# Performance work log

Hardware: AMD Instinct MI355X
Metric: run time of the kernel (lower is better)

Reference implementation:

```python
import jax, jax.numpy as jnp
import numpy as np

D_MODEL = 256
D_INNER = 512          # expand * d_model
HEADDIM = 64
NHEADS = D_INNER // HEADDIM   # 8
NGROUPS = 1
D_STATE = 64
D_IN_PROJ = 2 * D_INNER + 2 * NGROUPS * D_STATE + NHEADS   # 1160
CONV_DIM = D_INNER + 2 * NGROUPS * D_STATE                  # 640
LN_EPS = 1e-5


def setup_inputs() -> dict:
    key = jax.random.key(0)
    ks = jax.random.split(key, 16)
    s = 0.02
    # dt_bias init as in torch code
    dt = jnp.exp(jax.random.uniform(ks[10], (NHEADS,)) * (np.log(0.1) - np.log(0.001)) + np.log(0.001))
    dt = jnp.clip(dt, 1e-4)
    dt_bias = dt + jnp.log(-jnp.expm1(-dt))
    A_log = jnp.log(jax.random.uniform(ks[11], (NHEADS,), minval=1.0, maxval=16.0))
    return {
        "u": jax.random.normal(ks[0], (4, 8192, D_MODEL), dtype=jnp.float32),
        "H": 64,
        "W": 128,
        "W_in": jax.random.normal(ks[1], (D_IN_PROJ, D_MODEL), dtype=jnp.float32) * s,
        "W_stereo": jax.random.normal(ks[2], (D_IN_PROJ, D_INNER), dtype=jnp.float32) * s,
        "conv_l_w": jax.random.normal(ks[3], (CONV_DIM, 1, 3, 3), dtype=jnp.float32) * 0.1,
        "conv_l_b": jax.random.normal(ks[4], (CONV_DIM,), dtype=jnp.float32) * 0.01,
        "conv_r_w": jax.random.normal(ks[5], (CONV_DIM, 1, 3, 3), dtype=jnp.float32) * 0.1,
        "conv_r_b": jax.random.normal(ks[6], (CONV_DIM,), dtype=jnp.float32) * 0.01,
        "conv_w": jax.random.normal(ks[7], (CONV_DIM, 1, 3, 3), dtype=jnp.float32) * 0.1,
        "conv_b": jax.random.normal(ks[8], (CONV_DIM,), dtype=jnp.float32) * 0.01,
        "dt_bias": dt_bias,
        "A_log": A_log,
        "D_l": jnp.ones((NHEADS,), dtype=jnp.float32),
        "D_r": jnp.ones((NHEADS,), dtype=jnp.float32),
        "D": jnp.ones((NHEADS,), dtype=jnp.float32),
        "ln_g": jnp.ones((D_INNER,), dtype=jnp.float32),
        "ln_b": jnp.zeros((D_INNER,), dtype=jnp.float32),
        "W_out": jax.random.normal(ks[9], (D_MODEL, D_INNER), dtype=jnp.float32) * s,
    }


def _dwconv(x, w, b):
    # x: (B, C, H, W); depthwise 3x3 conv, SAME padding ((d_conv-1)//2 = 1)
    y = jax.lax.conv_general_dilated(
        x, w, window_strides=(1, 1), padding='SAME',
        dimension_numbers=('NCHW', 'OIHW', 'NCHW'),
        feature_group_count=CONV_DIM)
    return y + b[None, :, None, None]


def _layernorm(x, g, b):
    mu = x.mean(-1, keepdims=True)
    var = x.var(-1, keepdims=True)
    return (x - mu) / jnp.sqrt(var + LN_EPS) * g + b


def _lin_attn(x, dt, A, Bm, Cm, Dp):
    # x: (b, l, d_inner), dt: (b, l, h), Bm/Cm: (b, l, d_state); ngroups == 1
    b, l, _ = x.shape
    xh = x.reshape(b, l, NHEADS, HEADDIM)              # V: (b, l, h, p)
    dA = -(dt[..., None] * A[None, None, :, None])     # ssd_positve_dA -> -dt*A, (b,l,h,1)
    KV = jnp.einsum('bls,blhp->bhsp', Bm, xh * dA)     # K^T @ V_scaled
    y = jnp.einsum('bls,bhsp->blhp', Cm, KV)           # Q @ KV
    y = y + xh * Dp[None, None, :, None]               # skip D
    return y.reshape(b, l, D_INNER)


def reference(u, H, W, W_in, W_stereo, conv_l_w, conv_l_b, conv_r_w, conv_r_b,
              conv_w, conv_b, dt_bias, A_log, D_l, D_r, D, ln_g, ln_b, W_out):
    batch, seqlen, _ = u.shape
    half = batch // 2
    silu = jax.nn.silu
    A = -jnp.exp(A_log)

    zxbcdt = u @ W_in.T                                             # (b, l, 1160)
    z, xBC, dt = jnp.split(zxbcdt, [D_INNER, D_INNER + CONV_DIM], axis=-1)
    dt = jax.nn.softplus(dt + dt_bias)                              # (b, l, h)

    xBC = xBC.reshape(batch, H, W, CONV_DIM).transpose(0, 3, 1, 2)  # NCHW
    xBC1 = silu(_dwconv(xBC[:half], conv_l_w, conv_l_b)).transpose(0, 2, 3, 1).reshape(half, H * W, CONV_DIM)
    xBC2 = silu(_dwconv(xBC[half:], conv_r_w, conv_r_b)).transpose(0, 2, 3, 1).reshape(half, H * W, CONV_DIM)

    x1, B1, C1 = jnp.split(xBC1, [D_INNER, D_INNER + NGROUPS * D_STATE], axis=-1)
    x2, B2, C2 = jnp.split(xBC2, [D_INNER, D_INNER + NGROUPS * D_STATE], axis=-1)
    dt1, dt2 = dt[:half], dt[half:]

    y1 = _layernorm(_lin_attn(x1, dt1, A, B1, C1, D_l), ln_g, ln_b)
    y2 = _layernorm(_lin_attn(x2, dt2, A, B2, C2, D_r), ln_g, ln_b)
    y = jnp.concatenate([y1, y2], axis=0) * z

    zxs = y @ W_stereo.T
    zs, xBCs, dts = jnp.split(zxs, [D_INNER, D_INNER + CONV_DIM], axis=-1)
    dts = jax.nn.softplus(dts + dt_bias)

    xBCs = xBCs.reshape(batch, H, W, CONV_DIM).transpose(0, 3, 1, 2)
    xBCs = silu(_dwconv(xBCs, conv_w, conv_b)).transpose(0, 2, 3, 1).reshape(batch, H * W, CONV_DIM)
    xs, Bs, Cs = jnp.split(xBCs, [D_INNER, D_INNER + NGROUPS * D_STATE], axis=-1)

    ys = _layernorm(_lin_attn(xs, dts, A, Bs, Cs, D), ln_g, ln_b) * zs
    return ys @ W_out.T
```

## Files before the change

kernel.cpp:

```cpp
#include <hip/hip_runtime.h>
#include <hip/hip_bf16.h>
#include <math.h>

#define NB    4
#define LSEQ  8192
#define HH    64
#define WW    128
#define DMODEL 256
#define DINNER 512
#define NH    8
#define DSTATE 64
#define DPROJ 1160
#define CONVD 640
#define MROWS (NB*LSEQ)
#define KVCH  32
#define CBLK  80

typedef unsigned short bf16_t;
typedef __attribute__((ext_vector_type(8))) unsigned short ushort8v;
typedef __attribute__((ext_vector_type(8))) short short8v;
typedef __attribute__((ext_vector_type(4))) float f32x4;

static __device__ __forceinline__ float bf2f(bf16_t u) {
    return __uint_as_float(((unsigned)u) << 16);
}
static __device__ __forceinline__ bf16_t f2bf(float f) {
    unsigned u = __float_as_uint(f);
    u += 0x7FFFu + ((u >> 16) & 1u);
    return (bf16_t)(u >> 16);
}

template <typename TC>
__global__ __launch_bounds__(256) void gemm_mfma_bt(
    const bf16_t* __restrict__ A, int lda, size_t sAb,
    const bf16_t* __restrict__ B, int ldb, size_t sBb,
    TC* __restrict__ C, int ldc, size_t sCb,
    int M, int N, int K)
{
    __shared__ __align__(16) bf16_t As[128 * 32];
    __shared__ __align__(16) bf16_t Bs[128 * 32];
    const bf16_t* Ab = A + blockIdx.z * sAb;
    const bf16_t* Bb = B + blockIdx.z * sBb;
    TC*            Cb = C + blockIdx.z * sCb;
    const int tid = threadIdx.x;
    const int m0 = blockIdx.y * 128;
    const int n0 = blockIdx.x * 128;
    const int wid = tid >> 6;
    const int lane = tid & 63;
    const int wr = (wid >> 1) * 64;
    const int wc = (wid & 1) * 64;
    const int fr = lane & 15;
    const int fk = (lane >> 4) * 8;

    f32x4 acc[4][4];
    #pragma unroll
    for (int i = 0; i < 4; ++i)
        #pragma unroll
        for (int j = 0; j < 4; ++j) acc[i][j] = (f32x4){0.f, 0.f, 0.f, 0.f};

    const int srow = tid >> 2;
    const int scol = (tid & 3) * 8;
    const bf16_t* gA = Ab + (size_t)(m0 + srow) * lda + scol;
    const bf16_t* gB = Bb + (size_t)(n0 + srow) * ldb + scol;
    bf16_t* lA = As + tid * 8;
    bf16_t* lB = Bs + tid * 8;

    for (int k0 = 0; k0 < K; k0 += 32) {
        __builtin_amdgcn_global_load_lds(
            (const __attribute__((address_space(1))) void*)(gA + k0),
            (__attribute__((address_space(3))) void*)lA, 16, 0, 0);
        __builtin_amdgcn_global_load_lds(
            (const __attribute__((address_space(1))) void*)(gA + (size_t)64 * lda + k0),
            (__attribute__((address_space(3))) void*)(lA + 2048), 16, 0, 0);
        __builtin_amdgcn_global_load_lds(
            (const __attribute__((address_space(1))) void*)(gB + k0),
            (__attribute__((address_space(3))) void*)lB, 16, 0, 0);
        __builtin_amdgcn_global_load_lds(
            (const __attribute__((address_space(1))) void*)(gB + (size_t)64 * ldb + k0),
            (__attribute__((address_space(3))) void*)(lB + 2048), 16, 0, 0);
        __syncthreads();

        short8v a_frag[4], b_frag[4];
        #pragma unroll
        for (int m = 0; m < 4; ++m)
            a_frag[m] = *(const short8v*)&As[(wr + m * 16 + fr) * 32 + fk];
        #pragma unroll
        for (int n = 0; n < 4; ++n)
            b_frag[n] = *(const short8v*)&Bs[(wc + n * 16 + fr) * 32 + fk];
        #pragma unroll
        for (int m = 0; m < 4; ++m)
            #pragma unroll
            for (int n = 0; n < 4; ++n)
                acc[m][n] = __builtin_amdgcn_mfma_f32_16x16x32_bf16(
                    a_frag[m], b_frag[n], acc[m][n], 0, 0, 0);
        __syncthreads();
    }

    #pragma unroll
    for (int mi = 0; mi < 4; ++mi) {
        #pragma unroll
        for (int ni = 0; ni < 4; ++ni) {
            const int col = n0 + wc + ni * 16 + fr;
            if (col < N) {
                #pragma unroll
                for (int q = 0; q < 4; ++q) {
                    const int row = m0 + wr + mi * 16 + (lane >> 4) * 4 + q;
                    if constexpr (sizeof(TC) == 2)
                        Cb[(size_t)row * ldc + col] = f2bf(acc[mi][ni][q]);
                    else
                        Cb[(size_t)row * ldc + col] = acc[mi][ni][q];
                }
            }
        }
    }
}

__global__ __launch_bounds__(256) void cvt_bf16_kernel(
    const float* __restrict__ in, bf16_t* __restrict__ out, int n)
{
    const int base = (blockIdx.x * 256 + threadIdx.x) * 4;
    if (base >= n) return;
    float4 v = *(const float4*)&in[base];
    ushort4 o;
    o.x = f2bf(v.x); o.y = f2bf(v.y); o.z = f2bf(v.z); o.w = f2bf(v.w);
    *(ushort4*)&out[base] = o;
}

__global__ __launch_bounds__(256) void wpad_kernel(
    const float* __restrict__ W, bf16_t* __restrict__ Wp,
    int N, int Npad, int K)
{
    const int i = blockIdx.x * 256 + threadIdx.x;
    if (i >= Npad * K) return;
    const int r = i / K, k = i - r * K;
    Wp[i] = (r < N) ? f2bf(W[(size_t)r * K + k]) : (bf16_t)0;
}

__global__ __launch_bounds__(256) void dt_kernel(
    const bf16_t* __restrict__ zx, const float* __restrict__ dt_bias,
    float* __restrict__ dtbuf)
{
    const int idx = blockIdx.x * 256 + threadIdx.x;
    const int h = idx & 7;
    const int row = idx >> 3;
    const float v = bf2f(zx[(size_t)row * DPROJ + (DINNER + CONVD) + h]) + dt_bias[h];
    const float sp = (v > 0.f) ? (v + log1pf(expf(-v))) : log1pf(expf(v));
    dtbuf[idx] = sp;
}

__global__ __launch_bounds__(256) void conv_silu_kernel(
    const bf16_t* __restrict__ zx,
    const float* __restrict__ wA, const float* __restrict__ bA,
    const float* __restrict__ wB, const float* __restrict__ bB,
    bf16_t* __restrict__ out)
{
    const int idx = blockIdx.x * 256 + threadIdx.x;
    const int cb = idx % CBLK;
    const int t  = idx / CBLK;
    const int c0 = cb * 8;
    const int l = t & (LSEQ - 1);
    const int b = t >> 13;
    const int hh = l >> 7;
    const int ww = l & (WW - 1);
    const float* wp = (b < 2) ? wA : wB;
    const float* bp = (b < 2) ? bA : bB;

    float w[72];
    const float4* wsrc = (const float4*)(wp + c0 * 9);
    #pragma unroll
    for (int i = 0; i < 18; ++i) ((float4*)w)[i] = wsrc[i];

    float acc[8];
    float4 bv0 = *(const float4*)(bp + c0);
    float4 bv1 = *(const float4*)(bp + c0 + 4);
    acc[0] = bv0.x; acc[1] = bv0.y; acc[2] = bv0.z; acc[3] = bv0.w;
    acc[4] = bv1.x; acc[5] = bv1.y; acc[6] = bv1.z; acc[7] = bv1.w;

    const bf16_t* base = zx + (size_t)b * LSEQ * DPROJ + DINNER + c0;
    #pragma unroll
    for (int ki = -1; ki <= 1; ++ki) {
        const int hi = hh + ki;
        if ((unsigned)hi >= (unsigned)HH) continue;
        #pragma unroll
        for (int kj = -1; kj <= 1; ++kj) {
            const int wi = ww + kj;
            if ((unsigned)wi >= (unsigned)WW) continue;
            const ushort8v v = *(const ushort8v*)(base + (size_t)(hi * WW + wi) * DPROJ);
            const int tap = (ki + 1) * 3 + (kj + 1);
            #pragma unroll
            for (int q = 0; q < 8; ++q) acc[q] += bf2f(v[q]) * w[q * 9 + tap];
        }
    }
    ushort8v o;
    #pragma unroll
    for (int q = 0; q < 8; ++q) {
        const float s = acc[q] / (1.f + expf(-acc[q]));
        o[q] = f2bf(s);
    }
    *(ushort8v*)(out + (size_t)t * CONVD + c0) = o;
}

__global__ __launch_bounds__(128) void kv_part_kernel(
    const bf16_t* __restrict__ xconv, const float* __restrict__ dtbuf,
    const float* __restrict__ A_log, float* __restrict__ KVp)
{
    const int h = blockIdx.y, b = blockIdx.z, chunk = blockIdx.x;
    const int tid = threadIdx.x;
    const int w = tid >> 6, lane = tid & 63;
    __shared__ float lds[2 * 4352];
    float* Bt = lds + w * 4352;
    float* Xt = Bt + 2176;
    const float eA = expf(A_log[h]);
    const int s4  = (lane & 15) * 4;
    const int p16 = (lane >> 4) * 16;
    const int r    = lane & 31;
    const int part = lane >> 5;

    float acc[4][16];
    #pragma unroll
    for (int i = 0; i < 4; ++i)
        #pragma unroll
        for (int j = 0; j < 16; ++j) acc[i][j] = 0.f;

    const int l0 = b * LSEQ + chunk * 256;

    for (int t = 0; t < 8; t += 2) {
        const int row = l0 + (t + w) * 32 + r;
        const bf16_t* src = xconv + (size_t)row * CONVD + (part ? h * 64 : DINNER);
        const float scale = part ? dtbuf[row * NH + h] * eA : 1.f;
        float* dst = part ? &Xt[r * 68] : &Bt[r * 68];
        #pragma unroll
        for (int j = 0; j < 8; ++j) {
            ushort8v v = *(const ushort8v*)(src + j * 8);
            f32x4 lo = {bf2f(v[0]) * scale, bf2f(v[1]) * scale,
                        bf2f(v[2]) * scale, bf2f(v[3]) * scale};
            f32x4 hi = {bf2f(v[4]) * scale, bf2f(v[5]) * scale,
                        bf2f(v[6]) * scale, bf2f(v[7]) * scale};
            *(f32x4*)&dst[j * 8]     = lo;
            *(f32x4*)&dst[j * 8 + 4] = hi;
        }
        __syncthreads();
        #pragma unroll 4
        for (int rr = 0; rr < 32; ++rr) {
            const f32x4 bv = *(const f32x4*)&Bt[rr * 68 + s4];
            #pragma unroll
            for (int q = 0; q < 4; ++q) {
                const f32x4 xv = *(const f32x4*)&Xt[rr * 68 + p16 + q * 4];
                #pragma unroll
                for (int si = 0; si < 4; ++si)
                    #pragma unroll
                    for (int k = 0; k < 4; ++k)
                        acc[si][q * 4 + k] += bv[si] * xv[k];
            }
        }
        __syncthreads();
    }

    if (w == 0) {
        #pragma unroll
        for (int si = 0; si < 4; ++si)
            #pragma unroll
            for (int q = 0; q < 4; ++q)
                *(f32x4*)&lds[(s4 + si) * 68 + p16 + q * 4] =
                    (f32x4){acc[si][q*4], acc[si][q*4+1], acc[si][q*4+2], acc[si][q*4+3]};
    }
    __syncthreads();
    if (w == 1) {
        float* dst = KVp + ((size_t)chunk * (NB * NH) + (b * NH + h)) * 4096;
        #pragma unroll
        for (int si = 0; si < 4; ++si)
            #pragma unroll
            for (int q = 0; q < 4; ++q) {
                const f32x4 o = *(const f32x4*)&lds[(s4 + si) * 68 + p16 + q * 4];
                f32x4 v = {acc[si][q*4] + o[0], acc[si][q*4+1] + o[1],
                           acc[si][q*4+2] + o[2], acc[si][q*4+3] + o[3]};
                *(f32x4*)&dst[(s4 + si) * 64 + p16 + q * 4] = v;
            }
    }
}

__global__ __launch_bounds__(256) void kv_reduce_T_kernel(
    const float* __restrict__ KVp, bf16_t* __restrict__ KVT)
{
    const int idx = blockIdx.x * 256 + threadIdx.x;
    float s = 0.f;
    #pragma unroll
    for (int c = 0; c < KVCH; ++c) s += KVp[(size_t)c * 131072 + idx];
    const int bh = idx >> 12;
    const int ss = (idx >> 6) & 63;
    const int p  = idx & 63;
    KVT[((size_t)(bh * 64 + p)) * 64 + ss] = f2bf(s);
}

__global__ __launch_bounds__(256) void ln_gate_kernel(
    const bf16_t* __restrict__ Yattn, const bf16_t* __restrict__ xconv,
    const bf16_t* __restrict__ zx,
    const float* __restrict__ DA, const float* __restrict__ DB,
    const float* __restrict__ ln_g, const float* __restrict__ ln_b,
    bf16_t* __restrict__ ybuf)
{
    const int w = threadIdx.x >> 6, lane = threadIdx.x & 63;
    const int c0 = lane * 8;
    const int h = lane >> 3;
    float g[8], be[8];
    *(float4*)&g[0]  = *(const float4*)&ln_g[c0];
    *(float4*)&g[4]  = *(const float4*)&ln_g[c0 + 4];
    *(float4*)&be[0] = *(const float4*)&ln_b[c0];
    *(float4*)&be[4] = *(const float4*)&ln_b[c0 + 4];
    const int row0 = (blockIdx.x * 4 + w) * 4;

    for (int i = 0; i < 4; ++i) {
        const int row = row0 + i;
        const int b = row >> 13;
        const float Dv = (b < 2) ? DA[h] : DB[h];
        ushort8v yv = *(const ushort8v*)(Yattn + (size_t)row * DINNER + c0);
        ushort8v xv = *(const ushort8v*)(xconv + (size_t)row * CONVD + c0);
        float y[8];
        float s1 = 0.f, s2 = 0.f;
        #pragma unroll
        for (int q = 0; q < 8; ++q) {
            y[q] = bf2f(yv[q]) + bf2f(xv[q]) * Dv;
            s1 += y[q]; s2 += y[q] * y[q];
        }
        #pragma unroll
        for (int off = 32; off > 0; off >>= 1) {
            s1 += __shfl_xor(s1, off, 64);
            s2 += __shfl_xor(s2, off, 64);
        }
        const float mu = s1 * (1.f / 512.f);
        const float var = s2 * (1.f / 512.f) - mu * mu;
        const float rstd = rsqrtf(var + 1e-5f);
        ushort8v zv = *(const ushort8v*)(zx + (size_t)row * DPROJ + c0);
        ushort8v o;
        #pragma unroll
        for (int q = 0; q < 8; ++q)
            o[q] = f2bf(((y[q] - mu) * rstd * g[q] + be[q]) * bf2f(zv[q]));
        *(ushort8v*)(ybuf + (size_t)row * DINNER + c0) = o;
    }
}

extern "C" void kernel_launch(void* const* d_in, const int* in_sizes, int n_in,
                              void* d_out, int out_size, void* d_ws, size_t ws_size,
                              hipStream_t stream)
{
    const float* u        = (const float*)d_in[0];
    const float* W_in     = (const float*)d_in[3];
    const float* W_st     = (const float*)d_in[4];
    const float* conv_l_w = (const float*)d_in[5];
    const float* conv_l_b = (const float*)d_in[6];
    const float* conv_r_w = (const float*)d_in[7];
    const float* conv_r_b = (const float*)d_in[8];
    const float* conv_w   = (const float*)d_in[9];
    const float* conv_b   = (const float*)d_in[10];
    const float* dt_bias  = (const float*)d_in[11];
    const float* A_log    = (const float*)d_in[12];
    const float* D_l      = (const float*)d_in[13];
    const float* D_r      = (const float*)d_in[14];
    const float* Dp       = (const float*)d_in[15];
    const float* ln_g     = (const float*)d_in[16];
    const float* ln_b     = (const float*)d_in[17];
    const float* W_out    = (const float*)d_in[18];
    float* out = (float*)d_out;

    char* ws = (char*)d_ws;
    const size_t ZX_B    = (size_t)MROWS * DPROJ * 2;
    const size_t XCONV_B = (size_t)MROWS * CONVD * 2;
    const size_t YBUF_B  = (size_t)MROWS * DINNER * 2;
    const size_t DT_B    = (size_t)MROWS * NH * 4;
    const size_t KVT_B   = (size_t)NB * DINNER * 64 * 2;
    const size_t UBF_B   = (size_t)MROWS * DMODEL * 2;
    const size_t WIN_B   = (size_t)1280 * DMODEL * 2;
    const size_t WST_B   = (size_t)1280 * DINNER * 2;
    const size_t WOUT_B  = (size_t)256 * DINNER * 2;
    bf16_t* zx    = (bf16_t*)(ws);
    bf16_t* xconv = (bf16_t*)(ws + ZX_B);
    bf16_t* ybuf  = (bf16_t*)(ws + ZX_B + XCONV_B);
    float*  dtbuf = (float*) (ws + ZX_B + XCONV_B + YBUF_B);
    bf16_t* KVT   = (bf16_t*)(ws + ZX_B + XCONV_B + YBUF_B + DT_B);
    bf16_t* ubf   = (bf16_t*)(ws + ZX_B + XCONV_B + YBUF_B + DT_B + KVT_B);
    float*  KVp   = (float*) (ws + ZX_B + XCONV_B + YBUF_B + DT_B + KVT_B);
    bf16_t* WinP  = (bf16_t*)(ws + ZX_B + XCONV_B + YBUF_B + DT_B + KVT_B + UBF_B);
    bf16_t* WstP  = (bf16_t*)(ws + ZX_B + XCONV_B + YBUF_B + DT_B + KVT_B + UBF_B + WIN_B);
    bf16_t* WoutP = (bf16_t*)(ws + ZX_B + XCONV_B + YBUF_B + DT_B + KVT_B + UBF_B + WIN_B + WST_B);
    bf16_t* Yattn = (bf16_t*)(ws + ZX_B + XCONV_B + YBUF_B + DT_B + KVT_B + UBF_B + WIN_B + WST_B + WOUT_B);

    const dim3 gemmGridP(10, MROWS / 128);
    const dim3 gemmGridO(2,  MROWS / 128);
    const dim3 ymmGrid(4, LSEQ / 128, NB);
    const dim3 kvGrid(KVCH, NH, NB);
    const int convGrid = MROWS * CBLK / 256;
    const int lnGrid = MROWS / 16;

    cvt_bf16_kernel<<<(MROWS * DMODEL / 4 + 255) / 256, 256, 0, stream>>>(u, ubf, MROWS * DMODEL);
    wpad_kernel<<<(1280 * DMODEL + 255) / 256, 256, 0, stream>>>(W_in, WinP, DPROJ, 1280, DMODEL);
    wpad_kernel<<<(1280 * DINNER + 255) / 256, 256, 0, stream>>>(W_st, WstP, DPROJ, 1280, DINNER);
    wpad_kernel<<<(256 * DINNER + 255) / 256, 256, 0, stream>>>(W_out, WoutP, DMODEL, 256, DINNER);

    gemm_mfma_bt<bf16_t><<<gemmGridP, 256, 0, stream>>>(
        ubf, DMODEL, 0, WinP, DMODEL, 0, zx, DPROJ, 0, MROWS, DPROJ, DMODEL);
    dt_kernel<<<(MROWS * NH) / 256, 256, 0, stream>>>(zx, dt_bias, dtbuf);
    conv_silu_kernel<<<convGrid, 256, 0, stream>>>(
        zx, conv_l_w, conv_l_b, conv_r_w, conv_r_b, xconv);
    kv_part_kernel<<<kvGrid, 128, 0, stream>>>(xconv, dtbuf, A_log, KVp);
    kv_reduce_T_kernel<<<131072 / 256, 256, 0, stream>>>(KVp, KVT);
    gemm_mfma_bt<bf16_t><<<ymmGrid, 256, 0, stream>>>(
        xconv + DINNER + DSTATE, CONVD, (size_t)LSEQ * CONVD,
        KVT, 64, (size_t)DINNER * 64,
        Yattn, DINNER, (size_t)LSEQ * DINNER, LSEQ, DINNER, 64);
    ln_gate_kernel<<<lnGrid, 256, 0, stream>>>(
        Yattn, xconv, zx, D_l, D_r, ln_g, ln_b, ybuf);

    gemm_mfma_bt<bf16_t><<<gemmGridP, 256, 0, stream>>>(
        ybuf, DINNER, 0, WstP, DINNER, 0, zx, DPROJ, 0, MROWS, DPROJ, DINNER);
    dt_kernel<<<(MROWS * NH) / 256, 256, 0, stream>>>(zx, dt_bias, dtbuf);
    conv_silu_kernel<<<convGrid, 256, 0, stream>>>(
        zx, conv_w, conv_b, conv_w, conv_b, xconv);
    kv_part_kernel<<<kvGrid, 128, 0, stream>>>(xconv, dtbuf, A_log, KVp);
    kv_reduce_T_kernel<<<131072 / 256, 256, 0, stream>>>(KVp, KVT);
    gemm_mfma_bt<bf16_t><<<ymmGrid, 256, 0, stream>>>(
        xconv + DINNER + DSTATE, CONVD, (size_t)LSEQ * CONVD,
        KVT, 64, (size_t)DINNER * 64,
        Yattn, DINNER, (size_t)LSEQ * DINNER, LSEQ, DINNER, 64);
    ln_gate_kernel<<<lnGrid, 256, 0, stream>>>(
        Yattn, xconv, zx, Dp, Dp, ln_g, ln_b, ybuf);

    gemm_mfma_bt<float><<<gemmGridO, 256, 0, stream>>>(
        ybuf, DINNER, 0, WoutP, DINNER, 0, out, DMODEL, 0, MROWS, DMODEL, DINNER);
}
```

Before: 453.7 us.

## Add BK=64 MFMA GEMM with direct global-to-LDS loads and tile swizzle

Introduces a new GEMM kernel for the three projection matmuls. It uses a K-tile of 64, loads tiles straight from global memory into LDS with global_load_lds and an XOR-swizzled layout to avoid bank conflicts, and remaps workgroups for better L2 locality. It uses the 16x16x32 bf16 MFMA. The aim is fewer barriers per K and less register staging, at the cost of twice the LDS per block, which may lower occupancy.

After: 430.4 us. 1.05x faster.

```diff
diff --git a/kernel.cpp b/kernel.cpp
--- a/kernel.cpp
+++ b/kernel.cpp
@@ -28,6 +28,104 @@
     unsigned u = __float_as_uint(f);
     u += 0x7FFFu + ((u >> 16) & 1u);
     return (bf16_t)(u >> 16);
+}
+
+template <typename TC>
+__global__ __launch_bounds__(256) void gemm_mfma_bk64(
+    const bf16_t* __restrict__ A, int lda,
+    const bf16_t* __restrict__ B, int ldb,
+    TC* __restrict__ C, int ldc,
+    int M, int N, int K)
+{
+    __shared__ __align__(16) bf16_t As[128 * 64];
+    __shared__ __align__(16) bf16_t Bs[128 * 64];
+    const int nwg = gridDim.x * gridDim.y;
+    const int wg  = blockIdx.y * gridDim.x + blockIdx.x;
+    const int swz = (wg & 7) * (nwg >> 3) + (wg >> 3);
+    const int bx  = swz % gridDim.x;
+    const int by  = swz / gridDim.x;
+
+    const int tid = threadIdx.x;
+    const int m0 = by * 128;
+    const int n0 = bx * 128;
+    const int wid = tid >> 6;
+    const int lane = tid & 63;
+    const int wr = (wid >> 1) * 64;
+    const int wc = (wid & 1) * 64;
+    const int fr = lane & 15;
+    const int kq = lane >> 4;
+
+    f32x4 acc[4][4];
+    #pragma unroll
+    for (int i = 0; i < 4; ++i)
+        #pragma unroll
+        for (int j = 0; j < 4; ++j) acc[i][j] = (f32x4){0.f, 0.f, 0.f, 0.f};
+
+    const int lin0  = tid;
+    const int srow0 = lin0 >> 3;
+    const int sslot = lin0 & 7;
+
+    for (int k0 = 0; k0 < K; k0 += 64) {
+        #pragma unroll
+        for (int i = 0; i < 4; ++i) {
+            const int row  = srow0 + i * 32;
+            const int chunk = sslot ^ (row & 7);
+            const size_t ga = (size_t)(m0 + row) * lda + k0 + chunk * 8;
+            const size_t gb = (size_t)(n0 + row) * ldb + k0 + chunk * 8;
+            const int ldst = (i * 256 + tid) * 8;
+            __builtin_amdgcn_global_load_lds(
+                (const __attribute__((address_space(1))) void*)(A + ga),
+                (__attribute__((address_space(3))) void*)(As + ldst), 16, 0, 0);
+            __builtin_amdgcn_global_load_lds(
+                (const __attribute__((address_space(1))) void*)(B + gb),
+                (__attribute__((address_space(3))) void*)(Bs + ldst), 16, 0, 0);
+        }
+        __syncthreads();
+
+        short8v a_frag[2][4], b_frag[2][4];
+        #pragma unroll
+        for (int ks = 0; ks < 2; ++ks) {
+            #pragma unroll
+            for (int m = 0; m < 4; ++m) {
+                const int row = wr + m * 16 + fr;
+                const int slot = (ks * 4 + kq) ^ (fr & 7);
+                a_frag[ks][m] = *(const short8v*)&As[row * 64 + slot * 8];
+            }
+            #pragma unroll
+            for (int n = 0; n < 4; ++n) {
+                const int row = wc + n * 16 + fr;
+                const int slot = (ks * 4 + kq) ^ (fr & 7);
+                b_frag[ks][n] = *(const short8v*)&Bs[row * 64 + slot * 8];
+            }
+        }
+        #pragma unroll
+        for (int ks = 0; ks < 2; ++ks)
+            #pragma unroll
+            for (int m = 0; m < 4; ++m)
+                #pragma unroll
+                for (int n = 0; n < 4; ++n)
+                    acc[m][n] = __builtin_amdgcn_mfma_f32_16x16x32_bf16(
+                        a_frag[ks][m], b_frag[ks][n], acc[m][n], 0, 0, 0);
+        __syncthreads();
+    }
+
+    #pragma unroll
+    for (int mi = 0; mi < 4; ++mi) {
+        #pragma unroll
+        for (int ni = 0; ni < 4; ++ni) {
+            const int col = n0 + wc + ni * 16 + fr;
+            if (col < N) {
+                #pragma unroll
+                for (int q = 0; q < 4; ++q) {
+                    const int row = m0 + wr + mi * 16 + kq * 4 + q;
+                    if constexpr (sizeof(TC) == 2)
+                        C[(size_t)row * ldc + col] = f2bf(acc[mi][ni][q]);
+                    else
+                        C[(size_t)row * ldc + col] = acc[mi][ni][q];
+                }
+            }
+        }
+    }
 }
 
 template <typename TC>
@@ -396,8 +494,8 @@
     wpad_kernel<<<(1280 * DINNER + 255) / 256, 256, 0, stream>>>(W_st, WstP, DPROJ, 1280, DINNER);
     wpad_kernel<<<(256 * DINNER + 255) / 256, 256, 0, stream>>>(W_out, WoutP, DMODEL, 256, DINNER);
 
-    gemm_mfma_bt<bf16_t><<<gemmGridP, 256, 0, stream>>>(
-        ubf, DMODEL, 0, WinP, DMODEL, 0, zx, DPROJ, 0, MROWS, DPROJ, DMODEL);
+    gemm_mfma_bk64<bf16_t><<<gemmGridP, 256, 0, stream>>>(
+        ubf, DMODEL, WinP, DMODEL, zx, DPROJ, MROWS, DPROJ, DMODEL);
     dt_kernel<<<(MROWS * NH) / 256, 256, 0, stream>>>(zx, dt_bias, dtbuf);
     conv_silu_kernel<<<convGrid, 256, 0, stream>>>(
         zx, conv_l_w, conv_l_b, conv_r_w, conv_r_b, xconv);
@@ -410,8 +508,8 @@
     ln_gate_kernel<<<lnGrid, 256, 0, stream>>>(
         Yattn, xconv, zx, D_l, D_r, ln_g, ln_b, ybuf);
 
-    gemm_mfma_bt<bf16_t><<<gemmGridP, 256, 0, stream>>>(
-        ybuf, DINNER, 0, WstP, DINNER, 0, zx, DPROJ, 0, MROWS, DPROJ, DINNER);
+    gemm_mfma_bk64<bf16_t><<<gemmGridP, 256, 0, stream>>>(
+        ybuf, DINNER, WstP, DINNER, zx, DPROJ, MROWS, DPROJ, DINNER);
     dt_kernel<<<(MROWS * NH) / 256, 256, 0, stream>>>(zx, dt_bias, dtbuf);
     conv_silu_kernel<<<convGrid, 256, 0, stream>>>(
         zx, conv_w, conv_b, conv_w, conv_b, xconv);
@@ -424,6 +522,6 @@
     ln_gate_kernel<<<lnGrid, 256, 0, stream>>>(
         Yattn, xconv, zx, Dp, Dp, ln_g, ln_b, ybuf);
 
-    gemm_mfma_bt<float><<<gemmGridO, 256, 0, stream>>>(
-        ybuf, DINNER, 0, WoutP, DINNER, 0, out, DMODEL, 0, MROWS, DMODEL, DINNER);
-}
+    gemm_mfma_bk64<float><<<gemmGridO, 256, 0, stream>>>(
+        ybuf, DINNER, WoutP, DINNER, out, DMODEL, MROWS, DMODEL, DINNER);
+}
```
